# Kernel optimization log

Measured on AMD Instinct MI355X. Metric: run time of the kernel, lower is better.

The kernel has to match this reference:

```python
import jax, jax.numpy as jnp
import numpy as np

NEG_SLOPE = 0.01  # F.leaky_relu / nn.LeakyReLU default

def _leaky(x):
    return jnp.where(x >= 0, x, NEG_SLOPE * x)

def _cgconv(x, src, dst, edge_attr, Wf, bf, Ws, bs):
    # PyG CGConv: z = [x_i, x_j, e]; msg = sigmoid(lin_f(z)) * softplus(lin_s(z)); out = x + scatter_add(msg, i)
    z = jnp.concatenate([x[dst], x[src], edge_attr], axis=-1)  # [E, 2C+D]
    m = jax.nn.sigmoid(z @ Wf + bf) * jax.nn.softplus(z @ Ws + bs)  # [E, C]
    agg = jax.ops.segment_sum(m, dst, num_segments=x.shape[0])
    return x + agg

def setup_inputs() -> dict:
    key = jax.random.key(0)
    ks = jax.random.split(key, 16)
    N, E, C, D, NC, G = 50000, 800000, 128, 32, 10, 64
    inp = {}
    inp['x'] = jax.random.normal(ks[0], (N, C), dtype=jnp.float32)
    inp['y'] = jax.random.randint(ks[1], (G,), 0, NC)
    inp['edge_index'] = jax.random.randint(ks[2], (2, E), 0, N)
    inp['edge_attr'] = jax.random.normal(ks[3], (E, D), dtype=jnp.float32)
    inp['batch'] = jnp.sort(jax.random.randint(ks[4], (N,), 0, G))
    s = 0.05
    inp['lin_W'] = jax.random.normal(ks[5], (C + NC, C), dtype=jnp.float32) * s
    inp['lin_b'] = jnp.zeros((C,), dtype=jnp.float32)
    inp['c1_Wf'] = jax.random.normal(ks[6], (2 * C + D, C), dtype=jnp.float32) * s
    inp['c1_bf'] = jnp.zeros((C,), dtype=jnp.float32)
    inp['c1_Ws'] = jax.random.normal(ks[7], (2 * C + D, C), dtype=jnp.float32) * s
    inp['c1_bs'] = jnp.zeros((C,), dtype=jnp.float32)
    inp['c2_Wf'] = jax.random.normal(ks[8], (2 * C + D, C), dtype=jnp.float32) * s
    inp['c2_bf'] = jnp.zeros((C,), dtype=jnp.float32)
    inp['c2_Ws'] = jax.random.normal(ks[9], (2 * C + D, C), dtype=jnp.float32) * s
    inp['c2_bs'] = jnp.zeros((C,), dtype=jnp.float32)
    inp['fc1_W'] = jax.random.normal(ks[10], (C + NC, 32), dtype=jnp.float32) * s
    inp['fc1_b'] = jnp.zeros((32,), dtype=jnp.float32)
    inp['fc2_W'] = jax.random.normal(ks[11], (32, 1), dtype=jnp.float32) * s
    inp['fc2_b'] = jnp.zeros((1,), dtype=jnp.float32)
    return inp

def reference(x, y, edge_index, edge_attr, batch, lin_W, lin_b, c1_Wf, c1_bf, c1_Ws, c1_bs, c2_Wf, c2_bf, c2_Ws, c2_bs, fc1_W, fc1_b, fc2_W, fc2_b):
    NC = fc1_W.shape[0] - c1_Wf.shape[1]  # n_classes = 10
    G = y.shape[0]
    src, dst = edge_index[0], edge_index[1]
    one_hot = jax.nn.one_hot(y[batch], NC, dtype=x.dtype)  # [N, NC]
    h = _leaky(jnp.concatenate([x, one_hot], axis=1) @ lin_W + lin_b)
    h = _leaky(_cgconv(h, src, dst, edge_attr, c1_Wf, c1_bf, c1_Ws, c1_bs))
    h = _cgconv(h, src, dst, edge_attr, c2_Wf, c2_bf, c2_Ws, c2_bs)
    h = jnp.concatenate([h, one_hot], axis=1)  # [N, C+NC]
    sums = jax.ops.segment_sum(h, batch, num_segments=G)
    cnts = jax.ops.segment_sum(jnp.ones((h.shape[0],), h.dtype), batch, num_segments=G)
    pooled = sums / jnp.maximum(cnts, 1.0)[:, None]  # global_mean_pool
    out = _leaky(pooled @ fc1_W + fc1_b) @ fc2_W + fc2_b
    return jax.nn.sigmoid(out)
```

## Files before the change

### kernel.cpp

```cpp
#include <hip/hip_runtime.h>
#include <hip/hip_bf16.h>
#include <math.h>

#define CCH 128
#define DK  32
#define NCLS 10

__device__ __forceinline__ float leaky_f(float v) { return v >= 0.f ? v : 0.01f * v; }

__global__ void k_hist(const int* __restrict__ dst, int* __restrict__ cnt, int E) {
  int e = blockIdx.x * 256 + threadIdx.x;
  if (e < E) atomicAdd(&cnt[dst[e]], 1);
}

__global__ void k_scan(const int* __restrict__ cnt, int* __restrict__ off,
                       int* __restrict__ cur, int N) {
  __shared__ int wsum[16];
  __shared__ int carry_s;
  int t = threadIdx.x;
  int lane = t & 63, w = t >> 6;
  if (t == 0) carry_s = 0;
  __syncthreads();
  for (int base = 0; base < N; base += 1024) {
    int i = base + t;
    int carry = carry_s;
    int v = (i < N) ? cnt[i] : 0;
    int s = v;
    #pragma unroll
    for (int d = 1; d < 64; d <<= 1) {
      int tmp = __shfl_up(s, d);
      if (lane >= d) s += tmp;
    }
    if (lane == 63) wsum[w] = s;
    __syncthreads();
    if (t < 16) {
      int u = wsum[t];
      #pragma unroll
      for (int d = 1; d < 16; d <<= 1) {
        int tmp = __shfl_up(u, d);
        if (t >= d) u += tmp;
      }
      wsum[t] = u;
      if (t == 15) carry_s = carry + u;
    }
    __syncthreads();
    int wbase = carry + (w > 0 ? wsum[w - 1] : 0);
    int excl = wbase + s - v;
    if (i < N) { off[i] = excl; cur[i] = excl; }
    __syncthreads();
  }
  if (t == 0) off[N] = carry_s;
}

__global__ void k_fill(const int* __restrict__ dst, const int* __restrict__ srcArr,
                       int* __restrict__ cur, int* __restrict__ eid,
                       int* __restrict__ esrc, int E) {
  int e = blockIdx.x * 256 + threadIdx.x;
  if (e < E) {
    int p = atomicAdd(&cur[dst[e]], 1);
    eid[p] = e;
    esrc[p] = srcArr[e];
  }
}

__global__ __launch_bounds__(256) void k_embed(
    const float* __restrict__ x, const float* __restrict__ lin_W,
    const float* __restrict__ lin_b, const int* __restrict__ batch,
    const int* __restrict__ y, float* __restrict__ h, int M) {
  __shared__ float Al[32 * 128];
  __shared__ float Wl[32 * 128];
  int t = threadIdx.x;
  int row0 = blockIdx.x * 32;
  for (int i = t * 4; i < 32 * 128; i += 1024) {
    int r = i >> 7, k = i & 127;
    int gr = row0 + r;
    float4 v = {0.f, 0.f, 0.f, 0.f};
    if (gr < M) v = *(const float4*)&x[(size_t)gr * 128 + k];
    *(float4*)&Al[i] = v;
  }
  int c4 = (t & 31) * 4;
  int rb = (t >> 5) * 4;
  float acc[4][4] = {};
  for (int ks = 0; ks < 128; ks += 32) {
    __syncthreads();
    for (int i = t * 4; i < 32 * 128; i += 1024)
      *(float4*)&Wl[i] = *(const float4*)&lin_W[(size_t)ks * 128 + i];
    __syncthreads();
    for (int k = 0; k < 32; k += 4) {
      float4 a[4];
      #pragma unroll
      for (int r = 0; r < 4; ++r) a[r] = *(float4*)&Al[(rb + r) * 128 + ks + k];
      #pragma unroll
      for (int kk = 0; kk < 4; ++kk) {
        float4 w = *(float4*)&Wl[(k + kk) * 128 + c4];
        #pragma unroll
        for (int r = 0; r < 4; ++r) {
          float av = kk == 0 ? a[r].x : kk == 1 ? a[r].y : kk == 2 ? a[r].z : a[r].w;
          acc[r][0] = fmaf(av, w.x, acc[r][0]);
          acc[r][1] = fmaf(av, w.y, acc[r][1]);
          acc[r][2] = fmaf(av, w.z, acc[r][2]);
          acc[r][3] = fmaf(av, w.w, acc[r][3]);
        }
      }
    }
  }
  #pragma unroll
  for (int r = 0; r < 4; ++r) {
    int gr = row0 + rb + r;
    if (gr < M) {
      int cls = y[batch[gr]];
      const float* wrow = &lin_W[(size_t)(128 + cls) * 128];
      float4 o;
      o.x = leaky_f(acc[r][0] + lin_b[c4 + 0] + wrow[c4 + 0]);
      o.y = leaky_f(acc[r][1] + lin_b[c4 + 1] + wrow[c4 + 1]);
      o.z = leaky_f(acc[r][2] + lin_b[c4 + 2] + wrow[c4 + 2]);
      o.w = leaky_f(acc[r][3] + lin_b[c4 + 3] + wrow[c4 + 3]);
      *(float4*)&h[(size_t)gr * 128 + c4] = o;
    }
  }
}

__global__ __launch_bounds__(256) void k_proj(
    const float* __restrict__ h, const float* __restrict__ Wf,
    const float* __restrict__ Ws, float* __restrict__ P, int M) {
  __shared__ float Al[32 * 128];
  __shared__ float Wl[32 * 128];
  int t = threadIdx.x;
  int part = blockIdx.y;
  const float* Wsrc = (part < 2 ? Wf : Ws) + (size_t)(part & 1) * (128 * 128);
  int row0 = blockIdx.x * 32;
  for (int i = t * 4; i < 32 * 128; i += 1024) {
    int r = i >> 7, k = i & 127;
    int gr = row0 + r;
    float4 v = {0.f, 0.f, 0.f, 0.f};
    if (gr < M) v = *(const float4*)&h[(size_t)gr * 128 + k];
    *(float4*)&Al[i] = v;
  }
  int c4 = (t & 31) * 4;
  int rb = (t >> 5) * 4;
  float acc[4][4] = {};
  for (int ks = 0; ks < 128; ks += 32) {
    __syncthreads();
    for (int i = t * 4; i < 32 * 128; i += 1024)
      *(float4*)&Wl[i] = *(const float4*)&Wsrc[(size_t)ks * 128 + i];
    __syncthreads();
    for (int k = 0; k < 32; k += 4) {
      float4 a[4];
      #pragma unroll
      for (int r = 0; r < 4; ++r) a[r] = *(float4*)&Al[(rb + r) * 128 + ks + k];
      #pragma unroll
      for (int kk = 0; kk < 4; ++kk) {
        float4 w = *(float4*)&Wl[(k + kk) * 128 + c4];
        #pragma unroll
        for (int r = 0; r < 4; ++r) {
          float av = kk == 0 ? a[r].x : kk == 1 ? a[r].y : kk == 2 ? a[r].z : a[r].w;
          acc[r][0] = fmaf(av, w.x, acc[r][0]);
          acc[r][1] = fmaf(av, w.y, acc[r][1]);
          acc[r][2] = fmaf(av, w.z, acc[r][2]);
          acc[r][3] = fmaf(av, w.w, acc[r][3]);
        }
      }
    }
  }
  #pragma unroll
  for (int r = 0; r < 4; ++r) {
    int gr = row0 + rb + r;
    if (gr < M) {
      float4 o = {acc[r][0], acc[r][1], acc[r][2], acc[r][3]};
      *(float4*)&P[(size_t)gr * 512 + part * 128 + c4] = o;
    }
  }
}

__global__ __launch_bounds__(256, 2) void k_agg(
    const float* __restrict__ hin, const float* __restrict__ P,
    const int* __restrict__ off, const int* __restrict__ eidArr,
    const int* __restrict__ esrcArr, const float* __restrict__ ea,
    const float* __restrict__ Wf, const float* __restrict__ Ws,
    const float* __restrict__ bfv, const float* __restrict__ bsv,
    float* __restrict__ hout, int N, int do_leaky) {
  int lane = threadIdx.x & 63;
  int wave = __builtin_amdgcn_readfirstlane(threadIdx.x >> 6);
  int gw = blockIdx.x * 4 + wave;
  int half = gw & 1;
  int ch = half * 64 + lane;
  float wf[DK], ws[DK];
  #pragma unroll
  for (int k = 0; k < DK; ++k) {
    wf[k] = Wf[(size_t)(256 + k) * 128 + ch];
    ws[k] = Ws[(size_t)(256 + k) * 128 + ch];
  }
  #pragma unroll
  for (int k = 0; k < DK; ++k) {
    asm volatile("" : "+v"(wf[k]));
    asm volatile("" : "+v"(ws[k]));
  }
  float bf_c = bfv[ch], bs_c = bsv[ch];
  int nstreams = (gridDim.x * 4) >> 1;
  for (int n = gw >> 1; n < N; n += nstreams) {
    int i0 = __builtin_amdgcn_readfirstlane(off[n]);
    int i1 = __builtin_amdgcn_readfirstlane(off[n + 1]);
    float acc = hin[(size_t)n * 128 + ch];
    float gf0 = P[(size_t)n * 512 + ch] + bf_c;
    float gs0 = P[(size_t)n * 512 + 256 + ch] + bs_c;
    #pragma unroll 1
    for (int i = i0; i < i1; ++i) {
      int e = __builtin_amdgcn_readfirstlane(eidArr[i]);
      int s = __builtin_amdgcn_readfirstlane(esrcArr[i]);
      const float4* ep4 = (const float4*)(ea + (size_t)e * DK);
      float4 ev[DK / 4];
      #pragma unroll
      for (int q = 0; q < DK / 4; ++q) ev[q] = ep4[q];
      float gf = gf0 + P[(size_t)s * 512 + 128 + ch];
      float gs = gs0 + P[(size_t)s * 512 + 384 + ch];
      const float* evf = (const float*)ev;
      #pragma unroll
      for (int k = 0; k < DK; ++k) {
        float ek = evf[k];
        gf = fmaf(ek, wf[k], gf);
        gs = fmaf(ek, ws[k], gs);
      }
      float sg = 1.f / (1.f + __expf(-gf));
      float tt = __expf(-fabsf(gs));
      float sp = fmaxf(gs, 0.f) + __logf(1.f + tt);
      acc = fmaf(sg, sp, acc);
    }
    if (do_leaky) acc = leaky_f(acc);
    hout[(size_t)n * 128 + ch] = acc;
  }
}

__device__ __forceinline__ int lbound(const int* a, int n, int key) {
  int lo = 0, hi = n;
  while (lo < hi) { int m = (lo + hi) >> 1; if (a[m] < key) lo = m + 1; else hi = m; }
  return lo;
}

__global__ void k_pool(const float* __restrict__ h, const int* __restrict__ batch,
                       float* __restrict__ pooled, int* __restrict__ gcnt, int N) {
  int g = blockIdx.x;
  int sidx = blockIdx.y, sgrid = gridDim.y;
  int t = threadIdx.x;
  int lo = lbound(batch, N, g);
  int hi = lbound(batch, N, g + 1);
  int len = hi - lo;
  if (sidx == 0 && t == 0) gcnt[g] = len;
  int per = (len + sgrid - 1) / sgrid;
  int a = lo + sidx * per;
  int b = min(hi, a + per);
  if (a >= b) return;
  float s = 0.f;
  for (int n = a; n < b; ++n) s += h[(size_t)n * 128 + t];
  atomicAdd(&pooled[g * 128 + t], s);
}

__global__ void k_fc(const float* __restrict__ pooled, const int* __restrict__ gcnt,
                     const int* __restrict__ y,
                     const float* __restrict__ W1, const float* __restrict__ b1,
                     const float* __restrict__ W2, const float* __restrict__ b2,
                     float* __restrict__ out) {
  int g = blockIdx.x;
  int j = threadIdx.x;
  float v = 0.f;
  if (j < 32) {
    int cnt = gcnt[g];
    float dot = 0.f;
    for (int k = 0; k < 128; ++k) dot = fmaf(pooled[g * 128 + k], W1[k * 32 + j], dot);
    float a = b1[j] + (cnt > 0 ? dot / (float)cnt + W1[(128 + y[g]) * 32 + j] : 0.f);
    a = leaky_f(a);
    v = a * W2[j];
  }
  #pragma unroll
  for (int o = 32; o > 0; o >>= 1) v += __shfl_down(v, o);
  if (j == 0) out[g] = 1.f / (1.f + __expf(-(v + b2[0])));
}

extern "C" void kernel_launch(void* const* d_in, const int* in_sizes, int n_in,
                              void* d_out, int out_size, void* d_ws, size_t ws_size,
                              hipStream_t stream) {
  const float* x        = (const float*)d_in[0];
  const int*   y        = (const int*)d_in[1];
  const int*   eidx     = (const int*)d_in[2];
  const float* ea       = (const float*)d_in[3];
  const int*   batch    = (const int*)d_in[4];
  const float* lin_W    = (const float*)d_in[5];
  const float* lin_b    = (const float*)d_in[6];
  const float* c1_Wf    = (const float*)d_in[7];
  const float* c1_bf    = (const float*)d_in[8];
  const float* c1_Ws    = (const float*)d_in[9];
  const float* c1_bs    = (const float*)d_in[10];
  const float* c2_Wf    = (const float*)d_in[11];
  const float* c2_bf    = (const float*)d_in[12];
  const float* c2_Ws    = (const float*)d_in[13];
  const float* c2_bs    = (const float*)d_in[14];
  const float* fc1_W    = (const float*)d_in[15];
  const float* fc1_b    = (const float*)d_in[16];
  const float* fc2_W    = (const float*)d_in[17];
  const float* fc2_b    = (const float*)d_in[18];
  float* out = (float*)d_out;

  const int N = in_sizes[0] / 128;
  const int G = in_sizes[1];
  const int E = in_sizes[2] / 2;
  const int* src = eidx;
  const int* dst = eidx + E;

  char* w = (char*)d_ws;
  float* P  = (float*)w;  w += (size_t)N * 512 * 4;
  float* hA = (float*)w;  w += (size_t)N * 128 * 4;
  float* hB = (float*)w;  w += (size_t)N * 128 * 4;
  float* pooled = (float*)w; w += (size_t)G * 128 * 4;
  int* gcnt = (int*)w; w += ((size_t)G * 4 + 15) & ~(size_t)15;
  int* cnt = (int*)w; w += (size_t)N * 4;
  int* off = (int*)w; w += ((size_t)(N + 1) * 4 + 15) & ~(size_t)15;
  int* eid = (int*)w; w += (size_t)E * 4;
  int* esrc = (int*)w; w += (size_t)E * 4;

  hipMemsetAsync(cnt, 0, (size_t)N * 4, stream);
  hipMemsetAsync(pooled, 0, (size_t)G * 128 * 4, stream);
  k_hist<<<(E + 255) / 256, 256, 0, stream>>>(dst, cnt, E);
  k_scan<<<1, 1024, 0, stream>>>(cnt, off, cnt , N);
  k_fill<<<(E + 255) / 256, 256, 0, stream>>>(dst, src, cnt, eid, esrc, E);

  k_embed<<<(N + 31) / 32, 256, 0, stream>>>(x, lin_W, lin_b, batch, y, hA, N);

  k_proj<<<dim3((N + 31) / 32, 4), 256, 0, stream>>>(hA, c1_Wf, c1_Ws, P, N);
  k_agg<<<2048, 256, 0, stream>>>(hA, P, off, eid, esrc, ea, c1_Wf, c1_Ws, c1_bf, c1_bs, hB, N, 1);

  k_proj<<<dim3((N + 31) / 32, 4), 256, 0, stream>>>(hB, c2_Wf, c2_Ws, P, N);
  k_agg<<<2048, 256, 0, stream>>>(hB, P, off, eid, esrc, ea, c2_Wf, c2_Ws, c2_bf, c2_bs, hA, N, 0);

  k_pool<<<dim3(G, 8), 128, 0, stream>>>(hA, batch, pooled, gcnt, N);
  k_fc<<<G, 64, 0, stream>>>(pooled, gcnt, y, fc1_W, fc1_b, fc2_W, fc2_b, out);
}
```

Measured before the change: 1.275 ms.

## Process all 128 channels per wave in k_agg using packed float2 math

Each wave now handles a whole node, with each lane owning two adjacent channels held in float2 vectors, where before two waves split a node's channels in half. The per-edge index loads and the 32-float edge_attr reads are no longer duplicated across two waves, and the edge projection can use packed FMA (v_pk_fma_f32). Register use rises because the weight arrays double to 128 VGPRs, which may lower occupancy under launch_bounds(256,2), and each wave now carries twice the transcendental work.

```diff
diff --git a/kernel.cpp b/kernel.cpp
--- a/kernel.cpp
+++ b/kernel.cpp
@@ -5,6 +5,8 @@
 #define CCH 128
 #define DK  32
 #define NCLS 10
+
+typedef __attribute__((ext_vector_type(2))) float f32x2;
 
 __device__ __forceinline__ float leaky_f(float v) { return v >= 0.f ? v : 0.01f * v; }
 
@@ -182,27 +184,27 @@
   int lane = threadIdx.x & 63;
   int wave = __builtin_amdgcn_readfirstlane(threadIdx.x >> 6);
   int gw = blockIdx.x * 4 + wave;
-  int half = gw & 1;
-  int ch = half * 64 + lane;
-  float wf[DK], ws[DK];
+  int c2 = lane * 2;
+  f32x2 wf[DK], ws[DK];
   #pragma unroll
   for (int k = 0; k < DK; ++k) {
-    wf[k] = Wf[(size_t)(256 + k) * 128 + ch];
-    ws[k] = Ws[(size_t)(256 + k) * 128 + ch];
+    wf[k] = *(const f32x2*)&Wf[(size_t)(256 + k) * 128 + c2];
+    ws[k] = *(const f32x2*)&Ws[(size_t)(256 + k) * 128 + c2];
   }
   #pragma unroll
   for (int k = 0; k < DK; ++k) {
     asm volatile("" : "+v"(wf[k]));
     asm volatile("" : "+v"(ws[k]));
   }
-  float bf_c = bfv[ch], bs_c = bsv[ch];
-  int nstreams = (gridDim.x * 4) >> 1;
-  for (int n = gw >> 1; n < N; n += nstreams) {
+  f32x2 bf2 = *(const f32x2*)&bfv[c2];
+  f32x2 bs2 = *(const f32x2*)&bsv[c2];
+  int nstreams = gridDim.x * 4;
+  for (int n = gw; n < N; n += nstreams) {
     int i0 = __builtin_amdgcn_readfirstlane(off[n]);
     int i1 = __builtin_amdgcn_readfirstlane(off[n + 1]);
-    float acc = hin[(size_t)n * 128 + ch];
-    float gf0 = P[(size_t)n * 512 + ch] + bf_c;
-    float gs0 = P[(size_t)n * 512 + 256 + ch] + bs_c;
+    f32x2 acc = *(const f32x2*)&hin[(size_t)n * 128 + c2];
+    f32x2 gf0 = *(const f32x2*)&P[(size_t)n * 512 + c2] + bf2;
+    f32x2 gs0 = *(const f32x2*)&P[(size_t)n * 512 + 256 + c2] + bs2;
     #pragma unroll 1
     for (int i = i0; i < i1; ++i) {
       int e = __builtin_amdgcn_readfirstlane(eidArr[i]);
@@ -211,22 +213,25 @@
       float4 ev[DK / 4];
       #pragma unroll
       for (int q = 0; q < DK / 4; ++q) ev[q] = ep4[q];
-      float gf = gf0 + P[(size_t)s * 512 + 128 + ch];
-      float gs = gs0 + P[(size_t)s * 512 + 384 + ch];
+      f32x2 gf = gf0 + *(const f32x2*)&P[(size_t)s * 512 + 128 + c2];
+      f32x2 gs = gs0 + *(const f32x2*)&P[(size_t)s * 512 + 384 + c2];
       const float* evf = (const float*)ev;
       #pragma unroll
       for (int k = 0; k < DK; ++k) {
         float ek = evf[k];
-        gf = fmaf(ek, wf[k], gf);
-        gs = fmaf(ek, ws[k], gs);
+        f32x2 ek2 = {ek, ek};
+        gf += ek2 * wf[k];
+        gs += ek2 * ws[k];
       }
-      float sg = 1.f / (1.f + __expf(-gf));
-      float tt = __expf(-fabsf(gs));
-      float sp = fmaxf(gs, 0.f) + __logf(1.f + tt);
-      acc = fmaf(sg, sp, acc);
-    }
-    if (do_leaky) acc = leaky_f(acc);
-    hout[(size_t)n * 128 + ch] = acc;
+      float sgx = 1.f / (1.f + __expf(-gf.x));
+      float sgy = 1.f / (1.f + __expf(-gf.y));
+      float spx = fmaxf(gs.x, 0.f) + __logf(1.f + __expf(-fabsf(gs.x)));
+      float spy = fmaxf(gs.y, 0.f) + __logf(1.f + __expf(-fabsf(gs.y)));
+      acc.x = fmaf(sgx, spx, acc.x);
+      acc.y = fmaf(sgy, spy, acc.y);
+    }
+    if (do_leaky) { acc.x = leaky_f(acc.x); acc.y = leaky_f(acc.y); }
+    *(f32x2*)&hout[(size_t)n * 128 + c2] = acc;
   }
 }
 
```

Result: faster. 1.208 ms (-5.3%).
